# Kernel optimization log

Measured on AMD Instinct MI355X. Metric: run time of the kernel, lower is better.

The kernel has to match this reference:

```python
import jax, jax.numpy as jnp
import numpy as np
import math

B, N, D = 32, 1024, 512
S, R = 4, 64  # num_space, in_channels // reduction
EPS = 1e-12
COUNT = B  # self.count += b on first call
SCALE = 1.718 * math.exp(-COUNT / 30000.0) - 0.718


def sparsemax(z, axis=-1):
    # Martins & Astudillo sparsemax along `axis` (size K)
    K = z.shape[axis]
    z_sorted = -jnp.sort(-z, axis=axis)  # descending
    k = jnp.arange(1, K + 1, dtype=z.dtype).reshape((1,) * (z.ndim - 1) + (K,))
    k = jnp.moveaxis(k, -1, axis)
    z_cumsum = jnp.cumsum(z_sorted, axis=axis)
    support = (k * z_sorted > z_cumsum - 1).astype(z.dtype)
    k_sup = jnp.sum(support, axis=axis, keepdims=True)
    idx = (k_sup - 1).astype(jnp.int32)
    tau = (jnp.take_along_axis(z_cumsum, idx, axis=axis) - 1) / k_sup
    return jnp.maximum(z - tau, 0.0)


def setup_inputs() -> dict:
    key = jax.random.key(0)
    k1, k2, k3 = jax.random.split(key, 3)
    x = jax.random.normal(k1, (B, N, D), dtype=jnp.float32)
    mask = jax.random.randint(k2, (B,), 1, N + 1)  # valid token counts, >=1
    subspace = jax.random.normal(k3, (S, R, D), dtype=jnp.float32)
    return {"x": x, "mask": mask, "subspace": subspace}


def reference(x, mask, subspace):
    b, n, d = x.shape
    # BaseAggregator: L2-normalize tokens (F.normalize, p=2, dim=2)
    xn = x / jnp.maximum(jnp.linalg.norm(x, axis=2, keepdims=True), EPS)
    # project_matrix = subspace^T @ subspace / (d * scale); apply in two low-rank
    # steps to avoid per-token dxd matvec: y = S x, proj = S^T y
    y = jnp.einsum('skd,bnd->bnsk', subspace, xn)          # [b,n,S,R]
    proj = jnp.einsum('skd,bnsk->bnsd', subspace, y)       # [b,n,S,D]
    proj = proj / (d * SCALE)
    projection = jnp.linalg.norm(proj, axis=3)             # [b,n,S]
    probability = sparsemax(projection, axis=2)            # [b,n,S]
    max_indices = jnp.argmax(probability, axis=2)          # [b,n]
    # majority vote over valid tokens (bincount+argmax, vectorized)
    valid = (jnp.arange(n)[None, :] < mask[:, None])       # [b,n]
    onehot = jax.nn.one_hot(max_indices, S, dtype=jnp.float32) * valid[..., None]
    counts = onehot.sum(axis=1)                            # [b,S]
    vote = jnp.argmax(counts, axis=1)                      # [b]
    weights = jnp.take_along_axis(probability, vote[:, None, None], axis=2)[..., 0]  # [b,n]
    feature = jnp.sum(xn * weights[:, :, None], axis=1)    # [b,d]
    return feature
```

## Files before the change

### kernel.cpp

```cpp
#include <hip/hip_runtime.h>
#include <math.h>

#define BB 32
#define NN 1024
#define DD 512
#define SS 4
#define RR 64
#define OUTC 256
#define NT (BB*NN)
#define MT 64
#define NBLK (NT/MT)
#define BPB (NN/MT)

typedef float4 f4;
typedef float f32x4 __attribute__((ext_vector_type(4)));
typedef __bf16 bf16x8 __attribute__((ext_vector_type(8)));
typedef unsigned short u16x8 __attribute__((ext_vector_type(8)));

union BF8 { u16x8 u; bf16x8 b; unsigned w[4]; };

__device__ __forceinline__ float hif(float f) {
  return __uint_as_float(__float_as_uint(f) & 0xffff0000u);
}
__device__ __forceinline__ unsigned short topu(float f) {
  return (unsigned short)(__float_as_uint(f) >> 16);
}
__device__ __forceinline__ unsigned pack2(float e0, float e1) {
  return __builtin_amdgcn_perm(__float_as_uint(e1), __float_as_uint(e0), 0x07060302u);
}

#define MFMA(a,b,c) __builtin_amdgcn_mfma_f32_16x16x32_bf16((a),(b),(c),0,0,0)

#define BARRIER_LGKM() do { \
  asm volatile("s_waitcnt lgkmcnt(0)" ::: "memory"); \
  __builtin_amdgcn_s_barrier(); \
} while (0)

__global__ __launch_bounds__(256) void prep_kernel(const float* __restrict__ sub,
    unsigned short* __restrict__ subhi, unsigned short* __restrict__ sublo,
    unsigned short* __restrict__ Ghi, unsigned short* __restrict__ Glo) {
  int t = threadIdx.x, blk = blockIdx.x;
  __shared__ __align__(16) float Sl[64][36];
  if (blk < 128) {
    int i = (blk*256 + t)*4;
    f4 v = *(const f4*)&sub[i];
    uint2 hh, ll;
    hh.x = pack2(v.x, v.y); hh.y = pack2(v.z, v.w);
    ll.x = pack2(v.x - hif(v.x), v.y - hif(v.y));
    ll.y = pack2(v.z - hif(v.z), v.w - hif(v.w));
    *(uint2*)&subhi[i] = hh;
    *(uint2*)&sublo[i] = ll;
    return;
  }
  int s = blk - 128;
  int lane = t & 63, w = t >> 6, l15 = lane & 15, l4 = lane >> 4;
  int row = t >> 2, seg = t & 3;
  f4 r0, r1;
  f32x4 acc[4] = {{0,0,0,0},{0,0,0,0},{0,0,0,0},{0,0,0,0}};
  {
    const float* p = &sub[(size_t)(s*RR + row)*DD + seg*8];
    r0 = *(const f4*)p; r1 = *(const f4*)(p+4);
  }
  for (int kc = 0; kc < 16; ++kc) {
    __syncthreads();
    *(f4*)&Sl[row][seg*8]   = r0;
    *(f4*)&Sl[row][seg*8+4] = r1;
    __syncthreads();
    if (kc < 15) {
      const float* p = &sub[(size_t)(s*RR + row)*DD + (kc+1)*32 + seg*8];
      r0 = *(const f4*)p; r1 = *(const f4*)(p+4);
    }
    BF8 ah, al;
    {
      int ra = w*16 + l15;
      f32x4 v0 = *(const f32x4*)&Sl[ra][l4*8];
      f32x4 v1 = *(const f32x4*)&Sl[ra][l4*8+4];
      float ff[8] = {v0[0],v0[1],v0[2],v0[3],v1[0],v1[1],v1[2],v1[3]};
#pragma unroll
      for (int e = 0; e < 8; ++e) { ah.u[e] = topu(ff[e]); al.u[e] = topu(ff[e]-hif(ff[e])); }
    }
#pragma unroll
    for (int j = 0; j < 4; ++j) {
      BF8 bh, bl;
      int rb = j*16 + l15;
      f32x4 v0 = *(const f32x4*)&Sl[rb][l4*8];
      f32x4 v1 = *(const f32x4*)&Sl[rb][l4*8+4];
      float ff[8] = {v0[0],v0[1],v0[2],v0[3],v1[0],v1[1],v1[2],v1[3]};
#pragma unroll
      for (int e = 0; e < 8; ++e) { bh.u[e] = topu(ff[e]); bl.u[e] = topu(ff[e]-hif(ff[e])); }
      acc[j] = MFMA(ah.b, bh.b, acc[j]);
      acc[j] = MFMA(ah.b, bl.b, acc[j]);
      acc[j] = MFMA(al.b, bh.b, acc[j]);
    }
  }
#pragma unroll
  for (int j = 0; j < 4; ++j)
#pragma unroll
    for (int r = 0; r < 4; ++r) {
      int grow = w*16 + l4*4 + r, gcol = j*16 + l15;
      float v = acc[j][r];
      Ghi[((size_t)s*RR + grow)*RR + gcol] = topu(v);
      Glo[((size_t)s*RR + grow)*RR + gcol] = topu(v - hif(v));
    }
}

__global__ __launch_bounds__(512, 4) void fused_kernel(
    const float* __restrict__ x,
    const unsigned short* __restrict__ subhi, const unsigned short* __restrict__ sublo,
    const unsigned short* __restrict__ Ghi, const unsigned short* __restrict__ Glo,
    float inv_denom, int* __restrict__ amax, float* __restrict__ partial) {
  __shared__ __align__(16) unsigned short ldsA[2][2][64*40];
  __shared__ float ssqarr[64][8];
  __shared__ float prq2[64][4][2];
  __shared__ float Wl[64][4];

  int t = threadIdx.x;
  int lane = t & 63, w = t >> 6;
  int s = w & 3, ch = w >> 2;
  int l15 = lane & 15, l4 = lane >> 4;
  int m0 = blockIdx.x * MT;

  int srow = t >> 3, sseg = t & 7;
  const float* xrow = &x[(size_t)(m0 + srow)*DD + sseg*4];

  f32x4 acc[4][2] = {};
  float ssqp = 0.f;

  auto gload = [&](int kc) -> f4 {
    return *(const f4*)(xrow + kc*32);
  };
  auto cvtwrite = [&](int buf, f4 v) {
    float f0=v.x, f1=v.y, f2=v.z, f3=v.w;
    ssqp += f0*f0 + f1*f1 + f2*f2 + f3*f3;
    uint2 hh, ll;
    hh.x = pack2(f0,f1); hh.y = pack2(f2,f3);
    ll.x = pack2(f0-hif(f0), f1-hif(f1));
    ll.y = pack2(f2-hif(f2), f3-hif(f3));
    *(uint2*)&ldsA[buf][0][srow*40 + sseg*4] = hh;
    *(uint2*)&ldsA[buf][1][srow*40 + sseg*4] = ll;
  };
  auto loadB = [&](BF8 (&bh)[2], BF8 (&bl)[2], int kc) {
#pragma unroll
    for (int nf = 0; nf < 2; ++nf) {
      size_t off = (size_t)(s*64 + ch*32 + nf*16 + l15)*DD + kc*32 + l4*8;
      bh[nf].u = *(const u16x8*)&subhi[off];
      bl[nf].u = *(const u16x8*)&sublo[off];
    }
  };
  auto kstep = [&](int buf, BF8 (&bh)[2], BF8 (&bl)[2]) {
#pragma unroll
    for (int mf = 0; mf < 4; ++mf) {
      BF8 ah, al;
      int row = mf*16 + l15;
      ah.u = *(const u16x8*)&ldsA[buf][0][row*40 + l4*8];
      al.u = *(const u16x8*)&ldsA[buf][1][row*40 + l4*8];
#pragma unroll
      for (int nf = 0; nf < 2; ++nf) {
        acc[mf][nf] = MFMA(ah.b, bh[nf].b, acc[mf][nf]);
        acc[mf][nf] = MFMA(ah.b, bl[nf].b, acc[mf][nf]);
        acc[mf][nf] = MFMA(al.b, bh[nf].b, acc[mf][nf]);
      }
    }
  };

  BF8 bh0[2], bl0[2], bh1[2], bl1[2];
  {
    f4 r = gload(0);
    cvtwrite(0, r);
  }
  f4 rA = gload(1);
  f4 rB = gload(2);
  loadB(bh0, bl0, 0);
  for (int kc = 0; kc < 16; kc += 2) {
    BARRIER_LGKM();
    loadB(bh1, bl1, kc+1);
    cvtwrite(1, rA);
    if (kc < 14) rA = gload(kc+3);
    kstep(0, bh0, bl0);
    BARRIER_LGKM();
    if (kc < 14) {
      loadB(bh0, bl0, kc+2);
      cvtwrite(0, rB);
      if (kc < 12) rB = gload(kc+4);
    }
    kstep(1, bh1, bl1);
  }
  ssqarr[srow][sseg] = ssqp;

  BF8 gh[2][2], gl2[2][2];
#pragma unroll
  for (int kf = 0; kf < 2; ++kf)
#pragma unroll
    for (int nf = 0; nf < 2; ++nf) {
      size_t off = (size_t)(s*RR + (ch*2 + nf)*16 + l15)*RR + kf*32 + l4*8;
      gh[kf][nf].u  = *(const u16x8*)&Ghi[off];
      gl2[kf][nf].u = *(const u16x8*)&Glo[off];
    }
  float* ysc = (float*)&ldsA[0][0][0];

#pragma unroll
  for (int h = 0; h < 4; ++h) {
    __syncthreads();
#pragma unroll
    for (int nf = 0; nf < 2; ++nf)
#pragma unroll
      for (int r = 0; r < 4; ++r)
        ysc[s*1088 + (l4*4 + r)*68 + ch*32 + nf*16 + l15] = acc[h][nf][r];
    __syncthreads();
    BF8 yh[2], yl[2];
#pragma unroll
    for (int kf = 0; kf < 2; ++kf) {
      int base = s*1088 + l15*68 + kf*32 + l4*8;
      f32x4 v0 = *(const f32x4*)&ysc[base];
      f32x4 v1 = *(const f32x4*)&ysc[base+4];
      float ff[8] = {v0[0],v0[1],v0[2],v0[3],v1[0],v1[1],v1[2],v1[3]};
#pragma unroll
      for (int e = 0; e < 8; ++e) {
        yh[kf].u[e] = topu(ff[e]);
        yl[kf].u[e] = topu(ff[e] - hif(ff[e]));
      }
    }
    f32x4 z[2] = {};
#pragma unroll
    for (int nf = 0; nf < 2; ++nf)
#pragma unroll
      for (int kf = 0; kf < 2; ++kf) {
        z[nf] = MFMA(yh[kf].b, gh[kf][nf].b,  z[nf]);
        z[nf] = MFMA(yh[kf].b, gl2[kf][nf].b, z[nf]);
        z[nf] = MFMA(yl[kf].b, gh[kf][nf].b,  z[nf]);
      }
#pragma unroll
    for (int r = 0; r < 4; ++r) {
      float qp = z[0][r]*acc[h][0][r] + z[1][r]*acc[h][1][r];
      qp += __shfl_xor(qp, 1); qp += __shfl_xor(qp, 2);
      qp += __shfl_xor(qp, 4); qp += __shfl_xor(qp, 8);
      if (l15 == 0) prq2[h*16 + l4*4 + r][s][ch] = qp;
    }
  }
  __syncthreads();

  if (t < MT) {
    float ss = 0.f;
#pragma unroll
    for (int g = 0; g < 8; ++g) ss += ssqarr[t][g];
    float inv = 1.f / fmaxf(sqrtf(ss), 1e-12f);
    float p0 = sqrtf(fmaxf(prq2[t][0][0] + prq2[t][0][1], 0.f)) * inv * inv_denom;
    float p1 = sqrtf(fmaxf(prq2[t][1][0] + prq2[t][1][1], 0.f)) * inv * inv_denom;
    float p2 = sqrtf(fmaxf(prq2[t][2][0] + prq2[t][2][1], 0.f)) * inv * inv_denom;
    float p3 = sqrtf(fmaxf(prq2[t][3][0] + prq2[t][3][1], 0.f)) * inv * inv_denom;
    float a0=p0, a1=p1, a2=p2, a3=p3, hi, lo;
    hi = fmaxf(a0,a1); lo = fminf(a0,a1); a0=hi; a1=lo;
    hi = fmaxf(a2,a3); lo = fminf(a2,a3); a2=hi; a3=lo;
    hi = fmaxf(a0,a2); lo = fminf(a0,a2); a0=hi; a2=lo;
    hi = fmaxf(a1,a3); lo = fminf(a1,a3); a1=hi; a3=lo;
    hi = fmaxf(a1,a2); lo = fminf(a1,a2); a1=hi; a2=lo;
    float c2 = a0+a1, c3 = c2+a2, c4s = c3+a3;
    int ksup = 1 + (2.f*a1 > c2-1.f) + (3.f*a2 > c3-1.f) + (4.f*a3 > c4s-1.f);
    float csel = (ksup==1) ? a0 : (ksup==2) ? c2 : (ksup==3) ? c3 : c4s;
    float tau = (csel - 1.f) / (float)ksup;
    float q0 = fmaxf(p0-tau, 0.f), q1 = fmaxf(p1-tau, 0.f);
    float q2 = fmaxf(p2-tau, 0.f), q3 = fmaxf(p3-tau, 0.f);
    int arg = 0; float best = q0;
    if (q1 > best) { best = q1; arg = 1; }
    if (q2 > best) { best = q2; arg = 2; }
    if (q3 > best) { best = q3; arg = 3; }
    amax[m0 + t] = arg;
    Wl[t][0] = q0*inv; Wl[t][1] = q1*inv; Wl[t][2] = q2*inv; Wl[t][3] = q3*inv;
  }
  __syncthreads();

  {
    int grp = t >> 7, dcol = t & 127;
    f32x4 a0 = {0,0,0,0};
#pragma unroll 8
    for (int tok = 0; tok < MT; ++tok) {
      f32x4 v = *(const f32x4*)&x[(size_t)(m0 + tok)*DD + dcol*4];
      a0 += v * Wl[tok][grp];
    }
    *(f32x4*)&partial[((size_t)blockIdx.x*4 + grp)*DD + dcol*4] = a0;
  }
}

__global__ __launch_bounds__(256) void finish_kernel(const int* __restrict__ amax,
    const float* __restrict__ partial, const int* __restrict__ mask,
    float* __restrict__ out) {
  __shared__ int cnt[4];
  __shared__ int vsh;
  int bb = blockIdx.x, t = threadIdx.x;
  if (t < 4) cnt[t] = 0;
  __syncthreads();
  int m = mask[bb];
  int c0=0, c1=0, c2=0, c3=0;
  for (int n = t; n < NN; n += 256) {
    if (n < m) {
      int a = amax[bb*NN + n];
      c0 += (a==0); c1 += (a==1); c2 += (a==2); c3 += (a==3);
    }
  }
  atomicAdd(&cnt[0], c0); atomicAdd(&cnt[1], c1);
  atomicAdd(&cnt[2], c2); atomicAdd(&cnt[3], c3);
  __syncthreads();
  if (t == 0) {
    int arg = 0, best = cnt[0];
    if (cnt[1] > best) { best = cnt[1]; arg = 1; }
    if (cnt[2] > best) { best = cnt[2]; arg = 2; }
    if (cnt[3] > best) { best = cnt[3]; arg = 3; }
    vsh = arg;
  }
  __syncthreads();
  int v = vsh;
  for (int d = t; d < DD; d += 256) {
    float f = 0.f;
#pragma unroll
    for (int c = 0; c < BPB; ++c)
      f += partial[(((size_t)(bb*BPB + c))*4 + v)*DD + d];
    out[bb*DD + d] = f;
  }
}

extern "C" void kernel_launch(void* const* d_in, const int* in_sizes, int n_in,
                              void* d_out, int out_size, void* d_ws, size_t ws_size,
                              hipStream_t stream) {
  const float* x    = (const float*)d_in[0];
  const int*   mask = (const int*)d_in[1];
  const float* sub  = (const float*)d_in[2];
  float* out = (float*)d_out;

  float* partial = (float*)d_ws;
  int*   amax    = (int*)(partial + (size_t)NBLK*4*DD);
  unsigned short* subhi = (unsigned short*)(amax + NT);
  unsigned short* sublo = subhi + OUTC*DD;
  unsigned short* Ghi   = sublo + OUTC*DD;
  unsigned short* Glo   = Ghi + SS*RR*RR;

  double scale = 1.718 * exp(-((double)BB) / 30000.0) - 0.718;
  float inv_denom = (float)(1.0 / ((double)DD * scale));

  prep_kernel<<<128 + SS, 256, 0, stream>>>(sub, subhi, sublo, Ghi, Glo);
  fused_kernel<<<NBLK, 512, 0, stream>>>(x, subhi, sublo, Ghi, Glo, inv_denom, amax, partial);
  finish_kernel<<<BB, 256, 0, stream>>>(amax, partial, mask, out);
}
```

Before: 79.46 us.

## Stage x tiles via direct global-to-LDS loads with 4-deep fp32 ring buffer

Replaces the register-staged x tile loads (global→regs→bf16 hi/lo split→LDS) with global_load_lds async copies of raw fp32 into a 4-slot XOR-swizzled LDS ring, prefetching three k-steps ahead with explicit vmcnt waits. The bf16 hi/lo split and the sum-of-squares are now computed by each wave when it reads its A fragments, with only wave 0 accumulating ssq. The goal is to hide global latency better and remove register staging. The cost is redundant conversion work across 8 waves, more LDS per block, and hand-tuned vmcnt counts that must match the issue order exactly.

```diff
diff --git a/kernel.cpp b/kernel.cpp
--- a/kernel.cpp
+++ b/kernel.cpp
@@ -16,6 +16,8 @@
 typedef float f32x4 __attribute__((ext_vector_type(4)));
 typedef __bf16 bf16x8 __attribute__((ext_vector_type(8)));
 typedef unsigned short u16x8 __attribute__((ext_vector_type(8)));
+typedef const __attribute__((address_space(1))) void GVoid;
+typedef __attribute__((address_space(3))) void LVoid;
 
 union BF8 { u16x8 u; bf16x8 b; unsigned w[4]; };
 
@@ -35,6 +37,7 @@
   asm volatile("s_waitcnt lgkmcnt(0)" ::: "memory"); \
   __builtin_amdgcn_s_barrier(); \
 } while (0)
+#define WAITV(N) asm volatile("s_waitcnt vmcnt(" #N ")" ::: "memory")
 
 __global__ __launch_bounds__(256) void prep_kernel(const float* __restrict__ sub,
     unsigned short* __restrict__ subhi, unsigned short* __restrict__ sublo,
@@ -109,8 +112,8 @@
     const unsigned short* __restrict__ subhi, const unsigned short* __restrict__ sublo,
     const unsigned short* __restrict__ Ghi, const unsigned short* __restrict__ Glo,
     float inv_denom, int* __restrict__ amax, float* __restrict__ partial) {
-  __shared__ __align__(16) unsigned short ldsA[2][2][64*40];
-  __shared__ float ssqarr[64][8];
+  __shared__ __align__(16) float stage4[4][2048];
+  __shared__ float ssqlds[64];
   __shared__ float prq2[64][4][2];
   __shared__ float Wl[64][4];
 
@@ -120,24 +123,14 @@
   int l15 = lane & 15, l4 = lane >> 4;
   int m0 = blockIdx.x * MT;
 
-  int srow = t >> 3, sseg = t & 7;
-  const float* xrow = &x[(size_t)(m0 + srow)*DD + sseg*4];
-
   f32x4 acc[4][2] = {};
-  float ssqp = 0.f;
-
-  auto gload = [&](int kc) -> f4 {
-    return *(const f4*)(xrow + kc*32);
-  };
-  auto cvtwrite = [&](int buf, f4 v) {
-    float f0=v.x, f1=v.y, f2=v.z, f3=v.w;
-    ssqp += f0*f0 + f1*f1 + f2*f2 + f3*f3;
-    uint2 hh, ll;
-    hh.x = pack2(f0,f1); hh.y = pack2(f2,f3);
-    ll.x = pack2(f0-hif(f0), f1-hif(f1));
-    ll.y = pack2(f2-hif(f2), f3-hif(f3));
-    *(uint2*)&ldsA[buf][0][srow*40 + sseg*4] = hh;
-    *(uint2*)&ldsA[buf][1][srow*40 + sseg*4] = ll;
+  float ssq4[4] = {0.f, 0.f, 0.f, 0.f};
+
+  int drow = t >> 3, dsp = t & 7;
+  const float* dsrc0 = &x[(size_t)(m0 + drow)*DD + (dsp ^ (drow & 7))*4];
+  auto stage = [&](int p) {
+    __builtin_amdgcn_global_load_lds((GVoid*)(dsrc0 + p*32),
+        (LVoid*)((char*)&stage4[p & 3][0] + t*16), 16, 0, 0);
   };
   auto loadB = [&](BF8 (&bh)[2], BF8 (&bl)[2], int kc) {
 #pragma unroll
@@ -147,13 +140,25 @@
       bl[nf].u = *(const u16x8*)&sublo[off];
     }
   };
-  auto kstep = [&](int buf, BF8 (&bh)[2], BF8 (&bl)[2]) {
+  auto kstep = [&](int p, BF8 (&bh)[2], BF8 (&bl)[2]) {
+    const char* base = (const char*)&stage4[p & 3][0];
 #pragma unroll
     for (int mf = 0; mf < 4; ++mf) {
+      int row = mf*16 + l15;
+      int ph0 = (2*l4) ^ (row & 7), ph1 = (2*l4 + 1) ^ (row & 7);
+      f32x4 v0 = *(const f32x4*)(base + row*128 + ph0*16);
+      f32x4 v1 = *(const f32x4*)(base + row*128 + ph1*16);
+      float f0=v0[0], f1=v0[1], f2=v0[2], f3=v0[3];
+      float g4=v1[0], g5=v1[1], g6=v1[2], g7=v1[3];
+      if (w == 0)
+        ssq4[mf] += f0*f0+f1*f1+f2*f2+f3*f3+g4*g4+g5*g5+g6*g6+g7*g7;
       BF8 ah, al;
-      int row = mf*16 + l15;
-      ah.u = *(const u16x8*)&ldsA[buf][0][row*40 + l4*8];
-      al.u = *(const u16x8*)&ldsA[buf][1][row*40 + l4*8];
+      ah.w[0] = pack2(f0,f1); ah.w[1] = pack2(f2,f3);
+      ah.w[2] = pack2(g4,g5); ah.w[3] = pack2(g6,g7);
+      al.w[0] = pack2(f0-hif(f0), f1-hif(f1));
+      al.w[1] = pack2(f2-hif(f2), f3-hif(f3));
+      al.w[2] = pack2(g4-hif(g4), g5-hif(g5));
+      al.w[3] = pack2(g6-hif(g6), g7-hif(g7));
 #pragma unroll
       for (int nf = 0; nf < 2; ++nf) {
         acc[mf][nf] = MFMA(ah.b, bh[nf].b, acc[mf][nf]);
@@ -163,29 +168,31 @@
     }
   };
 
-  BF8 bh0[2], bl0[2], bh1[2], bl1[2];
-  {
-    f4 r = gload(0);
-    cvtwrite(0, r);
-  }
-  f4 rA = gload(1);
-  f4 rB = gload(2);
-  loadB(bh0, bl0, 0);
-  for (int kc = 0; kc < 16; kc += 2) {
+  BF8 bh[2], bl[2];
+  loadB(bh, bl, 0);
+  stage(0); stage(1); stage(2);
+  WAITV(2);
+#pragma unroll
+  for (int p = 0; p < 16; ++p) {
     BARRIER_LGKM();
-    loadB(bh1, bl1, kc+1);
-    cvtwrite(1, rA);
-    if (kc < 14) rA = gload(kc+3);
-    kstep(0, bh0, bl0);
-    BARRIER_LGKM();
-    if (kc < 14) {
-      loadB(bh0, bl0, kc+2);
-      cvtwrite(0, rB);
-      if (kc < 12) rB = gload(kc+4);
-    }
-    kstep(1, bh1, bl1);
-  }
-  ssqarr[srow][sseg] = ssqp;
+    if (p + 3 < 16) stage(p + 3);
+    kstep(p, bh, bl);
+    if (p + 1 < 16) loadB(bh, bl, p + 1);
+    if      (p == 0)  WAITV(7);
+    else if (p == 1)  WAITV(10);
+    else if (p <= 12) WAITV(14);
+    else if (p == 13) WAITV(13);
+    else if (p == 14) WAITV(12);
+  }
+
+  if (w == 0) {
+#pragma unroll
+    for (int mf = 0; mf < 4; ++mf) {
+      float v = ssq4[mf];
+      v += __shfl_xor(v, 16); v += __shfl_xor(v, 32);
+      if (lane < 16) ssqlds[mf*16 + lane] = v;
+    }
+  }
 
   BF8 gh[2][2], gl2[2][2];
 #pragma unroll
@@ -196,11 +203,11 @@
       gh[kf][nf].u  = *(const u16x8*)&Ghi[off];
       gl2[kf][nf].u = *(const u16x8*)&Glo[off];
     }
-  float* ysc = (float*)&ldsA[0][0][0];
-
+  __syncthreads();
+
+  float* ysc = &stage4[0][0];
 #pragma unroll
   for (int h = 0; h < 4; ++h) {
-    __syncthreads();
 #pragma unroll
     for (int nf = 0; nf < 2; ++nf)
 #pragma unroll
@@ -236,13 +243,11 @@
       qp += __shfl_xor(qp, 4); qp += __shfl_xor(qp, 8);
       if (l15 == 0) prq2[h*16 + l4*4 + r][s][ch] = qp;
     }
-  }
-  __syncthreads();
+    __syncthreads();
+  }
 
   if (t < MT) {
-    float ss = 0.f;
-#pragma unroll
-    for (int g = 0; g < 8; ++g) ss += ssqarr[t][g];
+    float ss = ssqlds[t];
     float inv = 1.f / fmaxf(sqrtf(ss), 1e-12f);
     float p0 = sqrtf(fmaxf(prq2[t][0][0] + prq2[t][0][1], 0.f)) * inv * inv_denom;
     float p1 = sqrtf(fmaxf(prq2[t][1][0] + prq2[t][1][1], 0.f)) * inv * inv_denom;
```

Result: faster. 76.19 us (-4.1%).

## Process two K-chunks per barrier with deeper LDS buffering and padded stride

Applied to the files above, without the earlier changes.

Restructures the main GEMM loop so each iteration consumes two 32-wide K chunks from a 4-slot LDS ring instead of one, halving the number of block barriers. Global x loads are issued two chunks ahead, and sched_barrier hints pin the load and MFMA ordering. The LDS row stride changes from 40 to 44 halfwords, which needs split 8-byte reads, likely to avoid bank conflicts. The trade is more LDS use and more registers, which may lower occupancy under launch_bounds(512,4).

```diff
diff --git a/kernel.cpp b/kernel.cpp
--- a/kernel.cpp
+++ b/kernel.cpp
@@ -11,6 +11,10 @@
 #define MT 64
 #define NBLK (NT/MT)
 #define BPB (NN/MT)
+
+#define ASTR 44
+#define APLANE (64*ASTR)
+#define ABUF (2*APLANE)
 
 typedef float4 f4;
 typedef float f32x4 __attribute__((ext_vector_type(4)));
@@ -109,7 +113,7 @@
     const unsigned short* __restrict__ subhi, const unsigned short* __restrict__ sublo,
     const unsigned short* __restrict__ Ghi, const unsigned short* __restrict__ Glo,
     float inv_denom, int* __restrict__ amax, float* __restrict__ partial) {
-  __shared__ __align__(16) unsigned short ldsA[2][2][64*40];
+  __shared__ __align__(16) unsigned short ldsA[4*ABUF];
   __shared__ float ssqarr[64][8];
   __shared__ float prq2[64][4][2];
   __shared__ float Wl[64][4];
@@ -126,8 +130,8 @@
   f32x4 acc[4][2] = {};
   float ssqp = 0.f;
 
-  auto gload = [&](int kc) -> f4 {
-    return *(const f4*)(xrow + kc*32);
+  auto gload = [&](int c) -> f4 {
+    return *(const f4*)(xrow + c*32);
   };
   auto cvtwrite = [&](int buf, f4 v) {
     float f0=v.x, f1=v.y, f2=v.z, f3=v.w;
@@ -136,13 +140,14 @@
     hh.x = pack2(f0,f1); hh.y = pack2(f2,f3);
     ll.x = pack2(f0-hif(f0), f1-hif(f1));
     ll.y = pack2(f2-hif(f2), f3-hif(f3));
-    *(uint2*)&ldsA[buf][0][srow*40 + sseg*4] = hh;
-    *(uint2*)&ldsA[buf][1][srow*40 + sseg*4] = ll;
+    unsigned short* p = &ldsA[buf*ABUF + srow*ASTR + sseg*4];
+    *(uint2*)p = hh;
+    *(uint2*)(p + APLANE) = ll;
   };
-  auto loadB = [&](BF8 (&bh)[2], BF8 (&bl)[2], int kc) {
+  auto loadB = [&](BF8 (&bh)[2], BF8 (&bl)[2], int c) {
 #pragma unroll
     for (int nf = 0; nf < 2; ++nf) {
-      size_t off = (size_t)(s*64 + ch*32 + nf*16 + l15)*DD + kc*32 + l4*8;
+      size_t off = (size_t)(s*64 + ch*32 + nf*16 + l15)*DD + c*32 + l4*8;
       bh[nf].u = *(const u16x8*)&subhi[off];
       bl[nf].u = *(const u16x8*)&sublo[off];
     }
@@ -150,10 +155,15 @@
   auto kstep = [&](int buf, BF8 (&bh)[2], BF8 (&bl)[2]) {
 #pragma unroll
     for (int mf = 0; mf < 4; ++mf) {
+      int row = mf*16 + l15;
+      const unsigned short* p = &ldsA[buf*ABUF + row*ASTR + l4*8];
+      uint2 h0  = *(const uint2*)p;
+      uint2 h1  = *(const uint2*)(p + 4);
+      uint2 lo0 = *(const uint2*)(p + APLANE);
+      uint2 lo1 = *(const uint2*)(p + APLANE + 4);
       BF8 ah, al;
-      int row = mf*16 + l15;
-      ah.u = *(const u16x8*)&ldsA[buf][0][row*40 + l4*8];
-      al.u = *(const u16x8*)&ldsA[buf][1][row*40 + l4*8];
+      ah.w[0]=h0.x;  ah.w[1]=h0.y;  ah.w[2]=h1.x;  ah.w[3]=h1.y;
+      al.w[0]=lo0.x; al.w[1]=lo0.y; al.w[2]=lo1.x; al.w[3]=lo1.y;
 #pragma unroll
       for (int nf = 0; nf < 2; ++nf) {
         acc[mf][nf] = MFMA(ah.b, bh[nf].b, acc[mf][nf]);
@@ -163,27 +173,31 @@
     }
   };
 
-  BF8 bh0[2], bl0[2], bh1[2], bl1[2];
-  {
-    f4 r = gload(0);
-    cvtwrite(0, r);
-  }
-  f4 rA = gload(1);
-  f4 rB = gload(2);
-  loadB(bh0, bl0, 0);
-  for (int kc = 0; kc < 16; kc += 2) {
+  f4 xrA0 = gload(0), xrA1 = gload(1);
+  cvtwrite(0, xrA0); cvtwrite(1, xrA1);
+  f4 xrB0 = gload(2), xrB1 = gload(3);
+  BARRIER_LGKM();
+
+#pragma unroll
+  for (int i = 0; i < 8; ++i) {
+    const int cons = (i & 1) * 2;
+    const int wr   = cons ^ 2;
+    BF8 bhA[2], blA[2], bhB[2], blB[2];
+    loadB(bhA, blA, 2*i);
+    loadB(bhB, blB, 2*i + 1);
+    __builtin_amdgcn_sched_barrier(0);
+    if (i < 6) {
+      if ((i & 1) == 0) { xrA0 = gload(2*i + 4); xrA1 = gload(2*i + 5); }
+      else              { xrB0 = gload(2*i + 4); xrB1 = gload(2*i + 5); }
+    }
+    __builtin_amdgcn_sched_barrier(0);
+    kstep(cons,     bhA, blA);
+    kstep(cons + 1, bhB, blB);
+    if (i < 7) {
+      if ((i & 1) == 0) { cvtwrite(wr, xrB0); cvtwrite(wr + 1, xrB1); }
+      else              { cvtwrite(wr, xrA0); cvtwrite(wr + 1, xrA1); }
+    }
     BARRIER_LGKM();
-    loadB(bh1, bl1, kc+1);
-    cvtwrite(1, rA);
-    if (kc < 14) rA = gload(kc+3);
-    kstep(0, bh0, bl0);
-    BARRIER_LGKM();
-    if (kc < 14) {
-      loadB(bh0, bl0, kc+2);
-      cvtwrite(0, rB);
-      if (kc < 12) rB = gload(kc+4);
-    }
-    kstep(1, bh1, bl1);
   }
   ssqarr[srow][sseg] = ssqp;
 
@@ -196,11 +210,11 @@
       gh[kf][nf].u  = *(const u16x8*)&Ghi[off];
       gl2[kf][nf].u = *(const u16x8*)&Glo[off];
     }
-  float* ysc = (float*)&ldsA[0][0][0];
-
+  __syncthreads();
+
+  float* ysc = (float*)&ldsA[0];
 #pragma unroll
   for (int h = 0; h < 4; ++h) {
-    __syncthreads();
 #pragma unroll
     for (int nf = 0; nf < 2; ++nf)
 #pragma unroll
@@ -236,8 +250,8 @@
       qp += __shfl_xor(qp, 4); qp += __shfl_xor(qp, 8);
       if (l15 == 0) prq2[h*16 + l4*4 + r][s][ch] = qp;
     }
-  }
-  __syncthreads();
+    __syncthreads();
+  }
 
   if (t < MT) {
     float ss = 0.f;
```

Measured after the change: 81.36 us. 1.02x slower.
